# Kernel tuning notes

Hardware: AMD Instinct MI355X
Metric: run time of the kernel (lower is better)

The kernel has to match this reference:

```python
import jax, jax.numpy as jnp
import numpy as np

BLOCK = 128
QMAX = 127.0


def _quant_dequant_act(x2d):
    """Dynamic per-token, per-128-column-group INT8 quantize + dequantize.

    x2d: [T, K]. Groups of shape 1x128 along K (is_weight=False path).
    """
    T, K = x2d.shape
    xb = x2d.reshape(T, K // BLOCK, BLOCK)
    amax = jnp.max(jnp.abs(xb), axis=-1, keepdims=True)
    scale = jnp.where(amax > 0, amax / QMAX, 1.0)
    q = jnp.clip(jnp.round(xb / scale), -QMAX, QMAX)  # int8 values
    return (q * scale).reshape(T, K)


def _quant_dequant_weight(w):
    """128x128 blockwise INT8 quantize + dequantize (is_weight=True path).

    w: [O, K] with O, K multiples of 128.
    """
    O, K = w.shape
    wb = w.reshape(O // BLOCK, BLOCK, K // BLOCK, BLOCK)
    amax = jnp.max(jnp.abs(wb), axis=(1, 3), keepdims=True)
    scale = jnp.where(amax > 0, amax / QMAX, 1.0)
    q = jnp.clip(jnp.round(wb / scale), -QMAX, QMAX)
    return (q * scale).reshape(O, K)


def setup_inputs() -> dict:
    key = jax.random.key(0)
    k1, k2, k3 = jax.random.split(key, 3)
    B, S, K, O = 4, 2048, 4096, 11008
    x = jax.random.normal(k1, (B, S, K), dtype=jnp.float32)
    w = jax.random.normal(k2, (O, K), dtype=jnp.float32) * 0.02
    bias = jax.random.normal(k3, (O,), dtype=jnp.float32) * 0.01
    return {"x": x, "w": w, "bias": bias}


def reference(x, w, bias):
    """INT8Linear forward: dynamic per-token INT8 activation quantization +
    128x128 blockwise-scaled INT8 weight GEMM + bias.

    Because scales are constant within each (token-group x weight-block),
    the blockwise-scaled int8 GEMM is mathematically identical to
    dequantize-then-matmul, which is the efficient dense expression here.
    """
    in_shape = x.shape
    x2d = x.reshape(-1, in_shape[-1])        # [T, K]
    xdq = _quant_dequant_act(x2d)            # [T, K]
    wdq = _quant_dequant_weight(w)           # [O, K]
    y = jnp.einsum('tk,ok->to', xdq, wdq) + bias
    return y.reshape(*in_shape[:-1], w.shape[0])
```

## Files before the change

### kernel.cpp

```cpp
#include <hip/hip_runtime.h>
#include <hip/hip_bf16.h>
#include <stdint.h>

#define QMAXF 127.0f

typedef __attribute__((ext_vector_type(8))) short bf16x8;
typedef __attribute__((ext_vector_type(4))) float f32x4;

typedef __attribute__((address_space(1))) void gbl_void;
typedef __attribute__((address_space(3))) void lds_void;

__device__ __forceinline__ void gload_lds16(const void* g, void* l) {
    __builtin_amdgcn_global_load_lds((const gbl_void*)g, (lds_void*)l, 16, 0, 0);
}

__device__ __forceinline__ unsigned short f2bf(float f) {
    unsigned int u = __builtin_bit_cast(unsigned int, f);
    unsigned int r = (u + 0x7fffu + ((u >> 16) & 1u)) >> 16;
    return (unsigned short)r;
}

__global__ __launch_bounds__(256) void qd_x_kernel(const float* __restrict__ x,
                                                   unsigned short* __restrict__ xdq,
                                                   long ngroups) {
    long gw = ((long)blockIdx.x * blockDim.x + threadIdx.x) >> 6;
    int lane = threadIdx.x & 63;
    if (gw >= ngroups) return;

    float2 v = *(reinterpret_cast<const float2*>(x) + gw * 64 + lane);
    float a = fmaxf(fabsf(v.x), fabsf(v.y));
#pragma unroll
    for (int off = 32; off; off >>= 1) a = fmaxf(a, __shfl_xor(a, off));

    float scale = a > 0.f ? a / QMAXF : 1.f;
    float qx = fminf(fmaxf(rintf(v.x / scale), -QMAXF), QMAXF);
    float qy = fminf(fmaxf(rintf(v.y / scale), -QMAXF), QMAXF);
    unsigned int packed = (unsigned int)f2bf(qx * scale) | ((unsigned int)f2bf(qy * scale) << 16);
    reinterpret_cast<unsigned int*>(xdq)[gw * 64 + lane] = packed;
}

__global__ __launch_bounds__(256) void qd_w_kernel(const float* __restrict__ w,
                                                   unsigned short* __restrict__ wdq,
                                                   int K) {
    int kb = blockIdx.x, ob = blockIdx.y;
    size_t base = (size_t)ob * 128 * K + (size_t)kb * 128;
    int t = threadIdx.x;

    float4 v[16];
    float a = 0.f;
#pragma unroll
    for (int i = 0; i < 16; i++) {
        int f = i * 256 + t;
        int row = f >> 5, c4 = f & 31;
        v[i] = *reinterpret_cast<const float4*>(w + base + (size_t)row * K + c4 * 4);
        a = fmaxf(a, fmaxf(fmaxf(fabsf(v[i].x), fabsf(v[i].y)),
                           fmaxf(fabsf(v[i].z), fabsf(v[i].w))));
    }
#pragma unroll
    for (int off = 32; off; off >>= 1) a = fmaxf(a, __shfl_xor(a, off));

    __shared__ float red[4];
    if ((t & 63) == 0) red[t >> 6] = a;
    __syncthreads();
    a = fmaxf(fmaxf(red[0], red[1]), fmaxf(red[2], red[3]));

    float scale = a > 0.f ? a / QMAXF : 1.f;
#pragma unroll
    for (int i = 0; i < 16; i++) {
        int f = i * 256 + t;
        int row = f >> 5, c4 = f & 31;
        float q0 = fminf(fmaxf(rintf(v[i].x / scale), -QMAXF), QMAXF);
        float q1 = fminf(fmaxf(rintf(v[i].y / scale), -QMAXF), QMAXF);
        float q2 = fminf(fmaxf(rintf(v[i].z / scale), -QMAXF), QMAXF);
        float q3 = fminf(fmaxf(rintf(v[i].w / scale), -QMAXF), QMAXF);
        uint2 p;
        p.x = (unsigned int)f2bf(q0 * scale) | ((unsigned int)f2bf(q1 * scale) << 16);
        p.y = (unsigned int)f2bf(q2 * scale) | ((unsigned int)f2bf(q3 * scale) << 16);
        *reinterpret_cast<uint2*>(wdq + base + (size_t)row * K + c4 * 4) = p;
    }
}

#define GBM 256
#define GBN 256
#define GBK 64
#define TILE_SH (GBM * GBK)
#define SLOT_SH (2 * TILE_SH)

#define BAR()                              \
    do {                                   \
        asm volatile("" ::: "memory");     \
        __builtin_amdgcn_s_barrier();      \
        asm volatile("" ::: "memory");     \
    } while (0)
#define WAITL0()                                          \
    do {                                                  \
        asm volatile("s_waitcnt lgkmcnt(0)" ::: "memory");\
        __builtin_amdgcn_sched_barrier(0);                \
    } while (0)
#define WAITV4() asm volatile("s_waitcnt vmcnt(4)" ::: "memory")

__global__ __launch_bounds__(512, 1) void gemm8p_kernel(
    const unsigned short* __restrict__ A,
    const unsigned short* __restrict__ Bw,
    const float* __restrict__ bias,
    float* __restrict__ C,
    int M, int N, int K) {
    __shared__ alignas(16) unsigned short lds[2 * SLOT_SH];

    int nTn = N / GBN;
    int nwg = gridDim.x, wg = blockIdx.x;
    int swz = (nwg & 7) ? wg : ((wg & 7) * (nwg >> 3) + (wg >> 3));
    int mt = swz / nTn;
    int nt = swz - mt * nTn;

    int t = threadIdx.x, wid = t >> 6, lane = t & 63;
    int wm = wid >> 2, wn = wid & 3;
    int lr = lane & 15, lq = lane >> 4;

    const unsigned short* Abase = A + (size_t)mt * GBM * K;
    const unsigned short* Bbase = Bw + (size_t)nt * GBN * K;

    int r0 = t >> 3;
    int pc = t & 7;
    int c0 = pc ^ (r0 & 7);
    const unsigned short* Aln = Abase + (size_t)r0 * K + c0 * 8;
    const unsigned short* Bln = Bbase + (size_t)r0 * K + c0 * 8;

    auto STAGE = [&](int slot, int mat, int half, int kb) {
        const unsigned short* g = (mat ? Bln : Aln) + (size_t)half * 128 * K + kb;
        unsigned short* d = &lds[slot * SLOT_SH + mat * TILE_SH + (half * 1024 + t) * 8];
        gload_lds16(g, d);
        gload_lds16(g + (size_t)64 * K, d + 512 * 8);
    };

    int xo0 = lq ^ (lr & 7);
    int xo1 = (4 + lq) ^ (lr & 7);
    int offA[4][2], offB[2][2];
#pragma unroll
    for (int m = 0; m < 4; m++) {
        int row = wm * 128 + m * 16 + lr;
        offA[m][0] = (row * 8 + xo0) * 8;
        offA[m][1] = (row * 8 + xo1) * 8;
    }
#pragma unroll
    for (int n = 0; n < 2; n++) {
        int row = wn * 64 + n * 16 + lr;
        offB[n][0] = TILE_SH + (row * 8 + xo0) * 8;
        offB[n][1] = TILE_SH + (row * 8 + xo1) * 8;
    }

    f32x4 acc[8][4];
#pragma unroll
    for (int m = 0; m < 8; m++)
#pragma unroll
        for (int n = 0; n < 4; n++) acc[m][n] = (f32x4){0.f, 0.f, 0.f, 0.f};

    bf16x8 ar[8], b0[4], b1[4];

    auto LDA = [&](int slot, int mq) {
        int base = slot * SLOT_SH + mq * 4096;
#pragma unroll
        for (int m = 0; m < 4; m++)
#pragma unroll
            for (int kk = 0; kk < 2; kk++)
                ar[m * 2 + kk] = *reinterpret_cast<const bf16x8*>(&lds[base + offA[m][kk]]);
    };
    auto LDB = [&](int slot, int nq, bf16x8* b) {
        int base = slot * SLOT_SH + nq * 2048;
#pragma unroll
        for (int n = 0; n < 2; n++)
#pragma unroll
            for (int kk = 0; kk < 2; kk++)
                b[n * 2 + kk] = *reinterpret_cast<const bf16x8*>(&lds[base + offB[n][kk]]);
    };
    auto MMA = [&](int mq, int nq, bf16x8* b) {
        __builtin_amdgcn_s_setprio(1);
#pragma unroll
        for (int m = 0; m < 4; m++)
#pragma unroll
            for (int n = 0; n < 2; n++)
#pragma unroll
                for (int kk = 0; kk < 2; kk++)
                    acc[mq * 4 + m][nq * 2 + n] = __builtin_amdgcn_mfma_f32_16x16x32_bf16(
                        ar[m * 2 + kk], b[n * 2 + kk], acc[mq * 4 + m][nq * 2 + n], 0, 0, 0);
        __builtin_amdgcn_s_setprio(0);
    };

    int NTm1 = K / GBK - 1;
    int NI = (K / GBK) / 2;

    STAGE(0, 0, 0, 0);
    STAGE(0, 0, 1, 0);
    STAGE(0, 1, 0, 0);
    STAGE(0, 1, 1, 0);
    STAGE(1, 1, 0, GBK);
    STAGE(1, 1, 1, GBK);
    WAITV4();
    BAR();

    for (int i = 0; i < NI; ++i) {
        int kb1 = min(2 * i + 1, NTm1) * GBK;
        int kb2 = min(2 * i + 2, NTm1) * GBK;
        int kb3 = min(2 * i + 3, NTm1) * GBK;

        LDA(0, 0); LDB(0, 0, b0);
        STAGE(1, 0, 0, kb1);
        BAR(); WAITL0();
        MMA(0, 0, b0);
        BAR();
        LDB(0, 1, b1);
        STAGE(1, 0, 1, kb1);
        BAR(); WAITL0();
        MMA(0, 1, b1);
        BAR();
        LDA(0, 1);
        STAGE(0, 1, 0, kb2);
        BAR(); WAITL0();
        MMA(1, 0, b0);
        BAR();
        STAGE(0, 1, 1, kb2);
        BAR();
        __builtin_amdgcn_sched_barrier(0);
        MMA(1, 1, b1);
        WAITV4();
        BAR();
        LDA(1, 0); LDB(1, 0, b0);
        STAGE(0, 0, 0, kb2);
        BAR(); WAITL0();
        MMA(0, 0, b0);
        BAR();
        LDB(1, 1, b1);
        STAGE(0, 0, 1, kb2);
        BAR(); WAITL0();
        MMA(0, 1, b1);
        BAR();
        LDA(1, 1);
        STAGE(1, 1, 0, kb3);
        BAR(); WAITL0();
        MMA(1, 0, b0);
        BAR();
        STAGE(1, 1, 1, kb3);
        BAR();
        __builtin_amdgcn_sched_barrier(0);
        MMA(1, 1, b1);
        WAITV4();
        BAR();
    }

    float bvv[4];
#pragma unroll
    for (int n = 0; n < 4; n++) bvv[n] = bias[nt * GBN + wn * 64 + n * 16 + lr];

#pragma unroll
    for (int m = 0; m < 8; m++) {
#pragma unroll
        for (int r = 0; r < 4; r++) {
            size_t row = (size_t)(mt * GBM + wm * 128 + m * 16 + lq * 4 + r);
            float* Crow = C + row * N + nt * GBN + wn * 64 + lr;
#pragma unroll
            for (int n = 0; n < 4; n++) Crow[n * 16] = acc[m][n][r] + bvv[n];
        }
    }
}

extern "C" void kernel_launch(void* const* d_in, const int* in_sizes, int n_in,
                              void* d_out, int out_size, void* d_ws, size_t ws_size,
                              hipStream_t stream) {
    const float* x = (const float*)d_in[0];
    const float* w = (const float*)d_in[1];
    const float* bias = (const float*)d_in[2];
    float* y = (float*)d_out;

    int O = in_sizes[2];
    int K = in_sizes[1] / O;
    int T = in_sizes[0] / K;

    unsigned short* xdq = (unsigned short*)d_ws;
    size_t xbytes = ((size_t)T * K * 2 + 255) & ~(size_t)255;
    unsigned short* wdq = (unsigned short*)((char*)d_ws + xbytes);

    long ngroups = (long)T * (K / 128);
    qd_x_kernel<<<dim3((unsigned)((ngroups + 3) / 4)), dim3(256), 0, stream>>>(x, xdq, ngroups);
    qd_w_kernel<<<dim3(K / 128, O / 128), dim3(256), 0, stream>>>(w, wdq, K);

    int grid = (T / GBM) * (O / GBN);
    gemm8p_kernel<<<dim3(grid), dim3(512), 0, stream>>>(xdq, wdq, bias, y, T, O, K);
}
```

Measured before the change: 763.1 us.

## Double-buffer A fragments and prefetch LDS reads one MMA phase ahead

Splits the A register fragment into even and odd buffers and issues the LDS reads for the next MMA quadrant before the current MMA runs, so LDS latency overlaps with matrix math. It drops one barrier per phase and changes the global-load wait from vmcnt(4) to vmcnt(2) at different points, with reads of the next slot issued after the wait. The cost is higher register pressure from the extra fragment buffer and a riskier ordering of LDS reads against asynchronous stage writes into the same slots.

Measured after the change: 763.0 us. Within noise of the previous version (-0.0%).

```diff
diff --git a/kernel.cpp b/kernel.cpp
--- a/kernel.cpp
+++ b/kernel.cpp
@@ -97,7 +97,8 @@
         asm volatile("s_waitcnt lgkmcnt(0)" ::: "memory");\
         __builtin_amdgcn_sched_barrier(0);                \
     } while (0)
-#define WAITV4() asm volatile("s_waitcnt vmcnt(4)" ::: "memory")
+#define WAITV(n) asm volatile("s_waitcnt vmcnt(" #n ")" ::: "memory")
+#define SCHED0() __builtin_amdgcn_sched_barrier(0)
 
 __global__ __launch_bounds__(512, 1) void gemm8p_kernel(
     const unsigned short* __restrict__ A,
@@ -155,9 +156,9 @@
 #pragma unroll
         for (int n = 0; n < 4; n++) acc[m][n] = (f32x4){0.f, 0.f, 0.f, 0.f};
 
-    bf16x8 ar[8], b0[4], b1[4];
-
-    auto LDA = [&](int slot, int mq) {
+    bf16x8 arE[8], arO[8], b0[4], b1[4];
+
+    auto LD_A = [&](int slot, int mq, bf16x8* ar) {
         int base = slot * SLOT_SH + mq * 4096;
 #pragma unroll
         for (int m = 0; m < 4; m++)
@@ -165,7 +166,7 @@
             for (int kk = 0; kk < 2; kk++)
                 ar[m * 2 + kk] = *reinterpret_cast<const bf16x8*>(&lds[base + offA[m][kk]]);
     };
-    auto LDB = [&](int slot, int nq, bf16x8* b) {
+    auto LD_B = [&](int slot, int nq, bf16x8* b) {
         int base = slot * SLOT_SH + nq * 2048;
 #pragma unroll
         for (int n = 0; n < 2; n++)
@@ -173,7 +174,7 @@
             for (int kk = 0; kk < 2; kk++)
                 b[n * 2 + kk] = *reinterpret_cast<const bf16x8*>(&lds[base + offB[n][kk]]);
     };
-    auto MMA = [&](int mq, int nq, bf16x8* b) {
+    auto MMA = [&](int mq, int nq, bf16x8* ar, bf16x8* b) {
         __builtin_amdgcn_s_setprio(1);
 #pragma unroll
         for (int m = 0; m < 4; m++)
@@ -195,55 +196,65 @@
     STAGE(0, 1, 1, 0);
     STAGE(1, 1, 0, GBK);
     STAGE(1, 1, 1, GBK);
-    WAITV4();
+    WAITV(4);
     BAR();
+    LD_A(0, 0, arE);
+    LD_B(0, 0, b0);
 
     for (int i = 0; i < NI; ++i) {
         int kb1 = min(2 * i + 1, NTm1) * GBK;
         int kb2 = min(2 * i + 2, NTm1) * GBK;
         int kb3 = min(2 * i + 3, NTm1) * GBK;
 
-        LDA(0, 0); LDB(0, 0, b0);
+        WAITL0();
+        LD_B(0, 1, b1);
         STAGE(1, 0, 0, kb1);
-        BAR(); WAITL0();
-        MMA(0, 0, b0);
-        BAR();
-        LDB(0, 1, b1);
+        SCHED0();
+        MMA(0, 0, arE, b0);
+        BAR();
+        WAITL0();
+        LD_A(0, 1, arO);
         STAGE(1, 0, 1, kb1);
-        BAR(); WAITL0();
-        MMA(0, 1, b1);
-        BAR();
-        LDA(0, 1);
+        SCHED0();
+        MMA(0, 1, arE, b1);
+        BAR();
+        WAITL0();
         STAGE(0, 1, 0, kb2);
-        BAR(); WAITL0();
-        MMA(1, 0, b0);
-        BAR();
+        SCHED0();
+        MMA(1, 0, arO, b0);
+        WAITV(2);
+        BAR();
+        WAITL0();
+        LD_A(1, 0, arE);
+        LD_B(1, 0, b0);
         STAGE(0, 1, 1, kb2);
-        BAR();
-        __builtin_amdgcn_sched_barrier(0);
-        MMA(1, 1, b1);
-        WAITV4();
-        BAR();
-        LDA(1, 0); LDB(1, 0, b0);
+        SCHED0();
+        MMA(1, 1, arO, b1);
+        BAR();
+        WAITL0();
+        LD_B(1, 1, b1);
         STAGE(0, 0, 0, kb2);
-        BAR(); WAITL0();
-        MMA(0, 0, b0);
-        BAR();
-        LDB(1, 1, b1);
+        SCHED0();
+        MMA(0, 0, arE, b0);
+        BAR();
+        WAITL0();
+        LD_A(1, 1, arO);
         STAGE(0, 0, 1, kb2);
-        BAR(); WAITL0();
-        MMA(0, 1, b1);
-        BAR();
-        LDA(1, 1);
+        SCHED0();
+        MMA(0, 1, arE, b1);
+        BAR();
+        WAITL0();
         STAGE(1, 1, 0, kb3);
-        BAR(); WAITL0();
-        MMA(1, 0, b0);
-        BAR();
+        SCHED0();
+        MMA(1, 0, arO, b0);
+        WAITV(2);
+        BAR();
+        WAITL0();
+        LD_A(0, 0, arE);
+        LD_B(0, 0, b0);
         STAGE(1, 1, 1, kb3);
-        BAR();
-        __builtin_amdgcn_sched_barrier(0);
-        MMA(1, 1, b1);
-        WAITV4();
+        SCHED0();
+        MMA(1, 1, arO, b1);
         BAR();
     }
 
```
